# Kernel tuning notes

Measured on AMD Instinct MI355X. Metric: run time of the kernel, lower is better.

The kernel has to match this reference:

```python
import jax, jax.numpy as jnp
import numpy as np

# norse LIFCell defaults
DT = 1e-3
TAU_SYN_INV = 200.0   # 1 / 5e-3
TAU_MEM_INV = 100.0   # 1 / 1e-2
V_TH = 1.0
V_LEAK = 0.0
V_RESET = 0.0
ALPHA = 100.0         # superspike surrogate slope
BN_EPS = 1e-5

@jax.custom_vjp
def heaviside(x):
    return (x > 0).astype(x.dtype)

def _h_fwd(x):
    return (x > 0).astype(x.dtype), x

def _h_bwd(x, g):
    # superspike surrogate: d/dx H(x) ~ 1 / (alpha*|x| + 1)^2
    return (g / (ALPHA * jnp.abs(x) + 1.0) ** 2,)

heaviside.defvjp(_h_fwd, _h_bwd)

def _bn(x, g, b, m, v):
    # inference-mode BatchNorm1d with running stats
    return (x - m) * jax.lax.rsqrt(v + BN_EPS) * g + b

def _lif(inp, st):
    v, i = st
    v_dec = v + DT * TAU_MEM_INV * ((V_LEAK - v) + i)
    i_dec = i - DT * TAU_SYN_INV * i
    z = heaviside(v_dec - V_TH)
    v_new = (1.0 - z) * v_dec + z * V_RESET
    return z, (v_new, i_dec + inp)

B, F, T = 4096, 256, 100
H1, H2, H3, OUT = 128, 64, 32, 2

def setup_inputs():
    key = jax.random.key(0)
    ks = jax.random.split(key, 16)
    def lin(k, o, i):
        return jax.random.normal(k, (o, i), jnp.float32) / np.float32(np.sqrt(i))
    def bnp(k, n):
        k1, k2, k3, k4 = jax.random.split(k, 4)
        return (jax.random.normal(k1, (n,), jnp.float32) * 0.1 + 1.0,
                jax.random.normal(k2, (n,), jnp.float32) * 0.1,
                jax.random.normal(k3, (n,), jnp.float32) * 0.1,
                jax.random.uniform(k4, (n,), jnp.float32) + 0.5)
    bn0 = bnp(ks[0], F); bn1 = bnp(ks[1], H1); bn2 = bnp(ks[2], H2); bn3 = bnp(ks[3], H3)
    return {
        "spike_input": (jax.random.uniform(ks[4], (B, F, T)) < 0.2).astype(jnp.float32),
        "bn0_g": bn0[0], "bn0_b": bn0[1], "bn0_m": bn0[2], "bn0_v": bn0[3],
        "W1": lin(ks[5], H1, F), "b1": jnp.zeros((H1,), jnp.float32),
        "bn1_g": bn1[0], "bn1_b": bn1[1], "bn1_m": bn1[2], "bn1_v": bn1[3],
        "W2": lin(ks[6], H2, H1), "b2": jnp.zeros((H2,), jnp.float32),
        "bn2_g": bn2[0], "bn2_b": bn2[1], "bn2_m": bn2[2], "bn2_v": bn2[3],
        "W3": lin(ks[7], H3, H2), "b3": jnp.zeros((H3,), jnp.float32),
        "bn3_g": bn3[0], "bn3_b": bn3[1], "bn3_m": bn3[2], "bn3_v": bn3[3],
        "Wout": lin(ks[8], OUT, H3), "bout": jnp.zeros((OUT,), jnp.float32),
    }

def reference(spike_input, bn0_g, bn0_b, bn0_m, bn0_v,
              W1, b1, bn1_g, bn1_b, bn1_m, bn1_v,
              W2, b2, bn2_g, bn2_b, bn2_m, bn2_v,
              W3, b3, bn3_g, bn3_b, bn3_m, bn3_v,
              Wout, bout):
    bsz = spike_input.shape[0]
    dt = spike_input.dtype
    xt = jnp.transpose(spike_input, (2, 0, 1))  # [T, B, F]
    def zs(n):
        return (jnp.zeros((bsz, n), dt), jnp.zeros((bsz, n), dt))
    init = (zs(W1.shape[0]), zs(W2.shape[0]), zs(W3.shape[0]), zs(Wout.shape[0]),
            jnp.zeros((bsz, Wout.shape[0]), dt))
    def step(carry, x):
        st1, st2, st3, sto, acc = carry
        x = _bn(x, bn0_g, bn0_b, bn0_m, bn0_v)
        s1, st1 = _lif(_bn(x @ W1.T + b1, bn1_g, bn1_b, bn1_m, bn1_v), st1)
        s2, st2 = _lif(_bn(s1 @ W2.T + b2, bn2_g, bn2_b, bn2_m, bn2_v), st2)
        s3, st3 = _lif(_bn(s2 @ W3.T + b3, bn3_g, bn3_b, bn3_m, bn3_v), st3)
        so, sto = _lif(s3 @ Wout.T + bout, sto)
        return (st1, st2, st3, sto, acc + so), None
    carry, _ = jax.lax.scan(step, init, xt)
    return carry[4]  # [B, output_size] accumulated output spikes
```

## Files before the change

kernel.cpp:

```cpp
#include <hip/hip_runtime.h>
#include <stdint.h>

typedef unsigned int   uint32;
typedef unsigned short ushortT;
typedef short bf16x8 __attribute__((ext_vector_type(8)));
typedef float f32x4  __attribute__((ext_vector_type(4)));

#define T_REAL 100

#define W1S 0
#define W2S 98304
#define W3S 122880
#define WOS 129024
#define B1F 65280
#define B2F 65408
#define B3F 65472
#define BOF 65504

#define UB_BASE 33792
#define LDS_BYTES 68608

#define MFMA(a,b,c) __builtin_amdgcn_mfma_f32_16x16x32_bf16(a,b,c,0,0,0)

__device__ __forceinline__ ushortT bf16rne(float x) {
    uint32 u = __float_as_uint(x);
    return (ushortT)((u + 0x7FFFu + ((u >> 16) & 1u)) >> 16);
}

__device__ __forceinline__ void split3(float w, ushortT& a, ushortT& b, ushortT& c) {
    a = bf16rne(w); float fa = __uint_as_float((uint32)a << 16);
    float r1 = w - fa;
    b = bf16rne(r1); float fb = __uint_as_float((uint32)b << 16);
    float r2 = r1 - fb;
    c = bf16rne(r2);
}

__global__ void prep_w(const float* __restrict__ W1, const float* __restrict__ W2,
                       const float* __restrict__ W3, const float* __restrict__ Wo,
                       const float* __restrict__ bn0g, const float* __restrict__ bn0v,
                       const float* __restrict__ bn1g, const float* __restrict__ bn1v,
                       const float* __restrict__ bn2g, const float* __restrict__ bn2v,
                       const float* __restrict__ bn3g, const float* __restrict__ bn3v,
                       ushortT* __restrict__ wsS)
{
    int idx = blockIdx.x * 256 + threadIdx.x;
    float w; int base, size, off;
    if (idx < 32768) {
        int h = idx >> 8, f = idx & 255;
        float A = bn0g[f] / sqrtf(bn0v[f] + 1e-5f);
        float G = bn1g[h] / sqrtf(bn1v[h] + 1e-5f);
        w = W1[idx] * A * G; base = W1S; size = 32768; off = idx;
    } else if (idx < 40960) {
        int r = idx - 32768; int h = r >> 7;
        float G = bn2g[h] / sqrtf(bn2v[h] + 1e-5f);
        w = W2[r] * G; base = W2S; size = 8192; off = r;
    } else if (idx < 43008) {
        int r = idx - 40960; int h = r >> 6;
        float G = bn3g[h] / sqrtf(bn3v[h] + 1e-5f);
        w = W3[r] * G; base = W3S; size = 2048; off = r;
    } else if (idx < 43520) {
        int r = idx - 43008; int o = r >> 5, k = r & 31;
        w = (o < 2) ? Wo[o * 32 + k] : 0.f;
        base = WOS; size = 512; off = r;
    } else return;
    ushortT a, b, c; split3(w, a, b, c);
    wsS[base + off] = a; wsS[base + size + off] = b; wsS[base + 2 * size + off] = c;
}

__global__ void prep_bias(const float* __restrict__ bn0g, const float* __restrict__ bn0b,
                          const float* __restrict__ bn0m, const float* __restrict__ bn0v,
                          const float* __restrict__ b1,   const float* __restrict__ W1,
                          const float* __restrict__ bn1g, const float* __restrict__ bn1b,
                          const float* __restrict__ bn1m, const float* __restrict__ bn1v,
                          const float* __restrict__ b2,   const float* __restrict__ bn2g,
                          const float* __restrict__ bn2b, const float* __restrict__ bn2m,
                          const float* __restrict__ bn2v,
                          const float* __restrict__ b3,   const float* __restrict__ bn3g,
                          const float* __restrict__ bn3b, const float* __restrict__ bn3m,
                          const float* __restrict__ bn3v,
                          const float* __restrict__ bo,   float* __restrict__ wsF)
{
    __shared__ float Cs[256];
    const int tid = threadIdx.x;
    {
        float A = bn0g[tid] / sqrtf(bn0v[tid] + 1e-5f);
        Cs[tid] = bn0b[tid] - bn0m[tid] * A;
    }
    __syncthreads();
    if (tid < 128) {
        float G  = bn1g[tid] / sqrtf(bn1v[tid] + 1e-5f);
        float Bn = bn1b[tid] - bn1m[tid] * G;
        float s  = b1[tid];
        const float* wr = W1 + tid * 256;
        for (int f = 0; f < 256; ++f) s = fmaf(wr[f], Cs[f], s);
        wsF[B1F + tid] = G * s + Bn;
    }
    if (tid < 64) {
        float G = bn2g[tid] / sqrtf(bn2v[tid] + 1e-5f);
        wsF[B2F + tid] = G * b2[tid] + (bn2b[tid] - bn2m[tid] * G);
    }
    if (tid < 32) {
        float G = bn3g[tid] / sqrtf(bn3v[tid] + 1e-5f);
        wsF[B3F + tid] = G * b3[tid] + (bn3b[tid] - bn3m[tid] * G);
    }
    if (tid < 2) wsF[BOF + tid] = bo[tid];
}

__global__ __launch_bounds__(256, 2) void snn_main(
    const float* __restrict__ xin,
    const ushortT* __restrict__ wsS,
    const float* __restrict__ wsF,
    float* __restrict__ out)
{
    __shared__ uint4 ldsq[LDS_BYTES / 16];
    char* lds = (char*)ldsq;
    char* xw = lds;
    char* s1 = lds;
    char* s2 = lds;
    char* s3 = lds;
    float* u1 = (float*)(lds + UB_BASE);
    float* u2 = u1;
    float* u3 = u1;
    float* uo = u1;

    const int tid  = threadIdx.x;
    const int lane = tid & 63;
    const int wv   = tid >> 6;
    const int wvu  = __builtin_amdgcn_readfirstlane(wv);
    const int lr   = lane & 15;
    const int lg   = lane >> 4;
    const int b0   = blockIdx.x * 4;

    const int gm = lane >> 2;
    const int gq = lane & 3;
    const float* xbase = xin + (size_t)(b0 + wvu) * 256 * 100;

    float4 xr[16];
#pragma unroll
    for (int i = 0; i < 16; ++i) {
        const int f = i * 16 + gm;
        xr[i] = *(const float4*)(xbase + f * 100 + gq * 4);
    }

    float v1a = 0, i1a = 0, v1b = 0, i1b = 0;
    float v2a = 0, i2a = 0, v2b = 0, i2b = 0;
    float v3a = 0, i3a = 0, v3b = 0, i3b = 0;
    float vo = 0, io = 0, aspk = 0;

#pragma unroll 1
    for (int w = 0; w < 7; ++w) {
        const int t0 = w * 16;
        __syncthreads();

#pragma unroll
        for (int i = 0; i < 16; ++i) {
            const int f = i * 16 + gm;
            char* colp = xw + f * 2;
            const int r0 = wvu * 16 + gq * 4;
            *(ushortT*)(colp + (size_t)(r0 + 0) * 528) = (ushortT)(__float_as_uint(xr[i].x) >> 16);
            *(ushortT*)(colp + (size_t)(r0 + 1) * 528) = (ushortT)(__float_as_uint(xr[i].y) >> 16);
            *(ushortT*)(colp + (size_t)(r0 + 2) * 528) = (ushortT)(__float_as_uint(xr[i].z) >> 16);
            *(ushortT*)(colp + (size_t)(r0 + 3) * 528) = (ushortT)(__float_as_uint(xr[i].w) >> 16);
        }
        __syncthreads();

        if (w < 6) {
            const int t0n = t0 + 16;
            const bool okq = (t0n + gq * 4) < T_REAL;
#pragma unroll
            for (int i = 0; i < 16; ++i) {
                const int f = i * 16 + gm;
                if (okq) xr[i] = *(const float4*)(xbase + f * 100 + t0n + gq * 4);
                else     xr[i] = make_float4(0.f, 0.f, 0.f, 0.f);
            }
        }

        {
            const int cb = wvu * 32;
            f32x4 acc[4][2];
            const float bia0 = wsF[B1F + cb + lr];
            const float bia1 = wsF[B1F + cb + 16 + lr];
#pragma unroll
            for (int rt = 0; rt < 4; ++rt) {
                acc[rt][0] = (f32x4){bia0, bia0, bia0, bia0};
                acc[rt][1] = (f32x4){bia1, bia1, bia1, bia1};
            }
#pragma unroll
            for (int ks = 0; ks < 8; ++ks) {
                const int koff = ks * 32 + lg * 8;
                const ushortT* wb0 = wsS + W1S + (cb + lr) * 256 + koff;
                const ushortT* wb1 = wb0 + 16 * 256;
                bf16x8 B00 = *(const bf16x8*)(wb0);
                bf16x8 B01 = *(const bf16x8*)(wb0 + 32768);
                bf16x8 B02 = *(const bf16x8*)(wb0 + 65536);
                bf16x8 B10 = *(const bf16x8*)(wb1);
                bf16x8 B11 = *(const bf16x8*)(wb1 + 32768);
                bf16x8 B12 = *(const bf16x8*)(wb1 + 65536);
#pragma unroll
                for (int rt = 0; rt < 4; ++rt) {
                    bf16x8 A = *(const bf16x8*)(xw + (size_t)(rt * 16 + lr) * 528 + koff * 2);
                    acc[rt][0] = MFMA(A, B00, acc[rt][0]);
                    acc[rt][1] = MFMA(A, B10, acc[rt][1]);
                    acc[rt][0] = MFMA(A, B01, acc[rt][0]);
                    acc[rt][1] = MFMA(A, B11, acc[rt][1]);
                    acc[rt][0] = MFMA(A, B02, acc[rt][0]);
                    acc[rt][1] = MFMA(A, B12, acc[rt][1]);
                }
            }
#pragma unroll
            for (int rt = 0; rt < 4; ++rt)
#pragma unroll
                for (int ct = 0; ct < 2; ++ct) {
                    float* up = u1 + (size_t)(rt * 128 + cb + ct * 16 + lr) * 17 + lg * 4;
#pragma unroll
                    for (int j = 0; j < 4; ++j) up[j] = acc[rt][ct][j];
                }
        }
        __syncthreads();

        {
            const float* uA = u1 + (size_t)(wvu * 128 + 2 * lane) * 17;
            const float* uB = uA + 17;
            char* dst = s1 + (size_t)(wvu * 16) * 272 + lane * 4;
            float vA = v1a, iA = i1a, vB = v1b, iB = i1b;
#pragma unroll
            for (int t = 0; t < 16; ++t) {
                float vdA = vA + 0.1f * ((0.0f - vA) + iA); bool zA = vdA > 1.0f;
                vA = zA ? 0.0f : vdA; iA = (iA - 0.2f * iA) + uA[t];
                float vdB = vB + 0.1f * ((0.0f - vB) + iB); bool zB = vdB > 1.0f;
                vB = zB ? 0.0f : vdB; iB = (iB - 0.2f * iB) + uB[t];
                *(uint32*)(dst + t * 272) = (zA ? 0x3F80u : 0u) | (zB ? 0x3F800000u : 0u);
            }
            v1a = vA; i1a = iA; v1b = vB; i1b = iB;
        }
        __syncthreads();

        {
            const int cb = wvu * 16;
            f32x4 acc[4];
            const float bia = wsF[B2F + cb + lr];
#pragma unroll
            for (int rt = 0; rt < 4; ++rt) acc[rt] = (f32x4){bia, bia, bia, bia};
#pragma unroll
            for (int ks = 0; ks < 4; ++ks) {
                const int koff = ks * 32 + lg * 8;
                const ushortT* wb = wsS + W2S + (cb + lr) * 128 + koff;
                bf16x8 Bh = *(const bf16x8*)(wb);
                bf16x8 Bm = *(const bf16x8*)(wb + 8192);
                bf16x8 Bl = *(const bf16x8*)(wb + 16384);
#pragma unroll
                for (int rt = 0; rt < 4; ++rt) {
                    bf16x8 A = *(const bf16x8*)(s1 + (size_t)(rt * 16 + lr) * 272 + koff * 2);
                    acc[rt] = MFMA(A, Bh, acc[rt]);
                    acc[rt] = MFMA(A, Bm, acc[rt]);
                    acc[rt] = MFMA(A, Bl, acc[rt]);
                }
            }
#pragma unroll
            for (int rt = 0; rt < 4; ++rt) {
                float* up = u2 + (size_t)(rt * 64 + cb + lr) * 17 + lg * 4;
#pragma unroll
                for (int j = 0; j < 4; ++j) up[j] = acc[rt][j];
            }
        }
        __syncthreads();

        if (lane < 32) {
            const float* uA = u2 + (size_t)(wvu * 64 + 2 * lane) * 17;
            const float* uB = uA + 17;
            char* dst = s2 + (size_t)(wvu * 16) * 144 + lane * 4;
            float vA = v2a, iA = i2a, vB = v2b, iB = i2b;
#pragma unroll
            for (int t = 0; t < 16; ++t) {
                float vdA = vA + 0.1f * ((0.0f - vA) + iA); bool zA = vdA > 1.0f;
                vA = zA ? 0.0f : vdA; iA = (iA - 0.2f * iA) + uA[t];
                float vdB = vB + 0.1f * ((0.0f - vB) + iB); bool zB = vdB > 1.0f;
                vB = zB ? 0.0f : vdB; iB = (iB - 0.2f * iB) + uB[t];
                *(uint32*)(dst + t * 144) = (zA ? 0x3F80u : 0u) | (zB ? 0x3F800000u : 0u);
            }
            v2a = vA; i2a = iA; v2b = vB; i2b = iB;
        }
        __syncthreads();

        {
            const int rhu = wvu >> 1, chu = wvu & 1;
            const int cb = chu * 16;
            f32x4 acc[2];
            const float bia = wsF[B3F + cb + lr];
            acc[0] = (f32x4){bia, bia, bia, bia};
            acc[1] = (f32x4){bia, bia, bia, bia};
#pragma unroll
            for (int ks = 0; ks < 2; ++ks) {
                const int koff = ks * 32 + lg * 8;
                const ushortT* wb = wsS + W3S + (cb + lr) * 64 + koff;
                bf16x8 Bh = *(const bf16x8*)(wb);
                bf16x8 Bm = *(const bf16x8*)(wb + 2048);
                bf16x8 Bl = *(const bf16x8*)(wb + 4096);
#pragma unroll
                for (int r = 0; r < 2; ++r) {
                    bf16x8 A = *(const bf16x8*)(s2 + (size_t)((rhu * 2 + r) * 16 + lr) * 144 + koff * 2);
                    acc[r] = MFMA(A, Bh, acc[r]);
                    acc[r] = MFMA(A, Bm, acc[r]);
                    acc[r] = MFMA(A, Bl, acc[r]);
                }
            }
#pragma unroll
            for (int r = 0; r < 2; ++r) {
                float* up = u3 + (size_t)((rhu * 2 + r) * 32 + cb + lr) * 17 + lg * 4;
#pragma unroll
                for (int j = 0; j < 4; ++j) up[j] = acc[r][j];
            }
        }
        __syncthreads();

        if (lane < 16) {
            const float* uA = u3 + (size_t)(wvu * 32 + 2 * lane) * 17;
            const float* uB = uA + 17;
            char* dst = s3 + (size_t)(wvu * 16) * 80 + lane * 4;
            float vA = v3a, iA = i3a, vB = v3b, iB = i3b;
#pragma unroll
            for (int t = 0; t < 16; ++t) {
                float vdA = vA + 0.1f * ((0.0f - vA) + iA); bool zA = vdA > 1.0f;
                vA = zA ? 0.0f : vdA; iA = (iA - 0.2f * iA) + uA[t];
                float vdB = vB + 0.1f * ((0.0f - vB) + iB); bool zB = vdB > 1.0f;
                vB = zB ? 0.0f : vdB; iB = (iB - 0.2f * iB) + uB[t];
                *(uint32*)(dst + t * 80) = (zA ? 0x3F80u : 0u) | (zB ? 0x3F800000u : 0u);
            }
            v3a = vA; i3a = iA; v3b = vB; i3b = iB;
        }
        __syncthreads();

        {
            const float bia = (lr < 2) ? wsF[BOF + lr] : 0.f;
            f32x4 acc = (f32x4){bia, bia, bia, bia};
            const int koff = lg * 8;
            const ushortT* wb = wsS + WOS + lr * 32 + koff;
            bf16x8 Bh = *(const bf16x8*)(wb);
            bf16x8 Bm = *(const bf16x8*)(wb + 512);
            bf16x8 Bl = *(const bf16x8*)(wb + 1024);
            bf16x8 A = *(const bf16x8*)(s3 + (size_t)(wvu * 16 + lr) * 80 + koff * 2);
            acc = MFMA(A, Bh, acc);
            acc = MFMA(A, Bm, acc);
            acc = MFMA(A, Bl, acc);
            if (lr < 2) {
                float* up = uo + (size_t)(wvu * 2 + lr) * 17 + lg * 4;
#pragma unroll
                for (int j = 0; j < 4; ++j) up[j] = acc[j];
            }
        }
        __syncthreads();

        if (tid < 8) {
            const float* ur = uo + tid * 17;
            float v = vo, ii = io, a = aspk;
#pragma unroll
            for (int t = 0; t < 16; ++t) {
                float vd = v + 0.1f * ((0.0f - v) + ii);
                bool z = vd > 1.0f; v = z ? 0.0f : vd;
                ii = (ii - 0.2f * ii) + ur[t];
                if (t0 + t < T_REAL) a += z ? 1.0f : 0.0f;
            }
            vo = v; io = ii; aspk = a;
        }
    }

    if (tid < 8) out[(size_t)(b0 + (tid >> 1)) * 2 + (tid & 1)] = aspk;
}

extern "C" void kernel_launch(void* const* d_in, const int* in_sizes, int n_in,
                              void* d_out, int out_size, void* d_ws, size_t ws_size,
                              hipStream_t stream)
{
    const float* x    = (const float*)d_in[0];
    const float* bn0g = (const float*)d_in[1];
    const float* bn0b = (const float*)d_in[2];
    const float* bn0m = (const float*)d_in[3];
    const float* bn0v = (const float*)d_in[4];
    const float* W1   = (const float*)d_in[5];
    const float* b1   = (const float*)d_in[6];
    const float* bn1g = (const float*)d_in[7];
    const float* bn1b = (const float*)d_in[8];
    const float* bn1m = (const float*)d_in[9];
    const float* bn1v = (const float*)d_in[10];
    const float* W2   = (const float*)d_in[11];
    const float* b2   = (const float*)d_in[12];
    const float* bn2g = (const float*)d_in[13];
    const float* bn2b = (const float*)d_in[14];
    const float* bn2m = (const float*)d_in[15];
    const float* bn2v = (const float*)d_in[16];
    const float* W3   = (const float*)d_in[17];
    const float* b3   = (const float*)d_in[18];
    const float* bn3g = (const float*)d_in[19];
    const float* bn3b = (const float*)d_in[20];
    const float* bn3m = (const float*)d_in[21];
    const float* bn3v = (const float*)d_in[22];
    const float* Wo   = (const float*)d_in[23];
    const float* bo   = (const float*)d_in[24];

    ushortT* wsS = (ushortT*)d_ws;
    float*   wsF = (float*)d_ws;
    float*   pout = (float*)d_out;

    prep_w<<<170, 256, 0, stream>>>(W1, W2, W3, Wo, bn0g, bn0v, bn1g, bn1v,
                                    bn2g, bn2v, bn3g, bn3v, wsS);
    prep_bias<<<1, 256, 0, stream>>>(bn0g, bn0b, bn0m, bn0v, b1, W1,
                                     bn1g, bn1b, bn1m, bn1v,
                                     b2, bn2g, bn2b, bn2m, bn2v,
                                     b3, bn3g, bn3b, bn3m, bn3v, bo, wsF);
    snn_main<<<1024, 256, 0, stream>>>(x, wsS, wsF, pout);
}
```

Baseline: 1.052 ms.

## Preload spike input as LDS bitmasks via ballot instead of per-window global loads

The kernel now reads each block's full spike input once at the start, thresholds every value with wave ballots, and stores the result as packed bitmasks in extra LDS. Each time window then expands these bits into bf16 1.0/0.0 tiles with 16-byte vectorized LDS writes, replacing the per-window prefetch of float4 registers and the scattered 2-byte stores. This removes 64 prefetch registers and the repeated strided global loads. In exchange, LDS use per block grows, which may lower occupancy, and the upfront load is no longer overlapped with compute. The threshold at 0.5 assumes the input contains only 0/1 spikes.

Result: no change. 1.036 ms (-1.6%).

```diff
diff --git a/kernel.cpp b/kernel.cpp
--- a/kernel.cpp
+++ b/kernel.cpp
@@ -18,7 +18,8 @@
 #define BOF 65504
 
 #define UB_BASE 33792
-#define LDS_BYTES 68608
+#define MK_BASE 68608
+#define LDS_BYTES 81408
 
 #define MFMA(a,b,c) __builtin_amdgcn_mfma_f32_16x16x32_bf16(a,b,c,0,0,0)
 
@@ -122,6 +123,7 @@
     float* u2 = u1;
     float* u3 = u1;
     float* uo = u1;
+    uint32* mk = (uint32*)(lds + MK_BASE);
 
     const int tid  = threadIdx.x;
     const int lane = tid & 63;
@@ -131,15 +133,27 @@
     const int lg   = lane >> 4;
     const int b0   = blockIdx.x * 4;
 
-    const int gm = lane >> 2;
-    const int gq = lane & 3;
-    const float* xbase = xin + (size_t)(b0 + wvu) * 256 * 100;
-
-    float4 xr[16];
-#pragma unroll
-    for (int i = 0; i < 16; ++i) {
-        const int f = i * 16 + gm;
-        xr[i] = *(const float4*)(xbase + f * 100 + gq * 4);
+    {
+        const int fg = wvu;
+        for (int s = 0; s < 4; ++s) {
+            const float* rp = xin + ((size_t)(b0 + s) * 256 + fg * 64 + lane) * T_REAL;
+            uint32* mrow = mk + (size_t)(s * 100) * 8 + fg * 2 + (lane >> 5);
+#pragma unroll 1
+            for (int q = 0; q < 25; ++q) {
+                float4 v = *(const float4*)(rp + q * 4);
+                unsigned long long bx = __ballot(v.x > 0.5f);
+                unsigned long long by = __ballot(v.y > 0.5f);
+                unsigned long long bz = __ballot(v.z > 0.5f);
+                unsigned long long bw = __ballot(v.w > 0.5f);
+                if ((lane & 31) == 0) {
+                    const int sh = (lane >> 5) * 32;
+                    mrow[(q * 4 + 0) * 8] = (uint32)(bx >> sh);
+                    mrow[(q * 4 + 1) * 8] = (uint32)(by >> sh);
+                    mrow[(q * 4 + 2) * 8] = (uint32)(bz >> sh);
+                    mrow[(q * 4 + 3) * 8] = (uint32)(bw >> sh);
+                }
+            }
+        }
     }
 
     float v1a = 0, i1a = 0, v1b = 0, i1b = 0;
@@ -153,27 +167,21 @@
         __syncthreads();
 
 #pragma unroll
-        for (int i = 0; i < 16; ++i) {
-            const int f = i * 16 + gm;
-            char* colp = xw + f * 2;
-            const int r0 = wvu * 16 + gq * 4;
-            *(ushortT*)(colp + (size_t)(r0 + 0) * 528) = (ushortT)(__float_as_uint(xr[i].x) >> 16);
-            *(ushortT*)(colp + (size_t)(r0 + 1) * 528) = (ushortT)(__float_as_uint(xr[i].y) >> 16);
-            *(ushortT*)(colp + (size_t)(r0 + 2) * 528) = (ushortT)(__float_as_uint(xr[i].z) >> 16);
-            *(ushortT*)(colp + (size_t)(r0 + 3) * 528) = (ushortT)(__float_as_uint(xr[i].w) >> 16);
-        }
-        __syncthreads();
-
-        if (w < 6) {
-            const int t0n = t0 + 16;
-            const bool okq = (t0n + gq * 4) < T_REAL;
-#pragma unroll
-            for (int i = 0; i < 16; ++i) {
-                const int f = i * 16 + gm;
-                if (okq) xr[i] = *(const float4*)(xbase + f * 100 + t0n + gq * 4);
-                else     xr[i] = make_float4(0.f, 0.f, 0.f, 0.f);
-            }
-        }
+        for (int j = 0; j < 8; ++j) {
+            const int c = tid + 256 * j;
+            const int r = c >> 5, g = c & 31;
+            const int s = r >> 4, tt = t0 + (r & 15);
+            const int ttc = (tt < T_REAL) ? tt : 0;
+            uint32 m = mk[(size_t)(s * 100 + ttc) * 8 + (g >> 2)];
+            m = (m >> ((g & 3) * 8)) & 0xFFu;
+            if (tt >= T_REAL) m = 0;
+            uint32 e0 = ((m & 1u)   ? 0x3F80u : 0u) | ((m & 2u)   ? 0x3F800000u : 0u);
+            uint32 e1 = ((m & 4u)   ? 0x3F80u : 0u) | ((m & 8u)   ? 0x3F800000u : 0u);
+            uint32 e2 = ((m & 16u)  ? 0x3F80u : 0u) | ((m & 32u)  ? 0x3F800000u : 0u);
+            uint32 e3 = ((m & 64u)  ? 0x3F80u : 0u) | ((m & 128u) ? 0x3F800000u : 0u);
+            *(uint4*)(xw + (size_t)r * 528 + g * 16) = make_uint4(e0, e1, e2, e3);
+        }
+        __syncthreads();
 
         {
             const int cb = wvu * 32;
```
